# Kernel tuning notes

Measured on AMD Instinct MI355X. Metric: run time of the kernel, lower is better.

Reference implementation:

```python
import jax, jax.numpy as jnp
import numpy as np

BINS = 10  # constructor default


def setup_inputs() -> dict:
    key = jax.random.key(0)
    k1, k2 = jax.random.split(key)
    bs, cla = 262144, 128
    # probabilities strictly inside (0,1) so log terms are finite
    u = jax.random.uniform(k1, (bs, cla), dtype=jnp.float32)
    inputs = 0.01 + 0.98 * u
    # binary 0/1 targets as floats
    targets = jnp.round(jax.random.uniform(k2, (bs, cla), dtype=jnp.float32))
    return {"inputs": inputs, "targets": targets}


def reference(inputs, targets):
    bins = BINS
    tot = jnp.asarray(inputs.size, jnp.float32)  # bs * cla

    # gradient-norm proxy g = |p.detach() - t|, in [0, 1]
    g = jnp.abs(jax.lax.stop_gradient(inputs) - targets)

    # edges are i/bins with the last edge nudged to 1+1e-6, so
    # floor(g*bins) clipped to bins-1 reproduces the per-bin masks exactly
    idx = jnp.clip(jnp.floor(g * bins).astype(jnp.int32), 0, bins - 1)

    # histogram counts per bin (fused scatter-add instead of the Python loop)
    counts = jnp.zeros((bins,), jnp.float32).at[idx.ravel()].add(1.0)

    n = jnp.sum(counts > 0).astype(jnp.float32)  # number of non-empty bins
    w_per_bin = jnp.where(counts > 0, tot / jnp.maximum(counts, 1.0), 0.0)
    weights = w_per_bin[idx] / jnp.maximum(n, 1.0)
    weights = jax.lax.stop_gradient(weights)  # weights built from detached g

    # elementwise binary cross entropy on probabilities
    bce = -(targets * jnp.log(inputs) + (1.0 - targets) * jnp.log1p(-inputs))
    loss = jnp.sum(weights * bce) / tot
    return loss
```

## Files before the change

kernel.cpp:

```cpp
#include <hip/hip_runtime.h>

#define BINS 10

__device__ __forceinline__ void elem(float p, float t,
                                     float* __restrict__ sb,
                                     unsigned int* __restrict__ cw)
{
    float g  = fabsf(p - t);
    float l2 = __log2f(1.0f - g);
    int   bi = (int)(g * 10.0f);
#pragma unroll
    for (int b = 0; b < BINS; ++b) {
        bool hit = (bi == b);
        unsigned long long m = __ballot(hit);
        sb[b] += hit ? l2 : 0.0f;
        cw[b] += (unsigned int)__popcll(m);
    }
}

__device__ __forceinline__ void proc4v(const float4 p, const float4 t,
                                       float* __restrict__ sb,
                                       unsigned int* __restrict__ cw)
{
    elem(p.x, t.x, sb, cw); elem(p.y, t.y, sb, cw);
    elem(p.z, t.z, sb, cw); elem(p.w, t.w, sb, cw);
}

__global__ __launch_bounds__(256, 4) void ghm_partial(
    const float4* __restrict__ p4,
    const float4* __restrict__ t4,
    float* __restrict__ gsum,
    unsigned int* __restrict__ gcnt,
    int n4)
{
    float        sb[BINS];
    unsigned int cw[BINS];
#pragma unroll
    for (int b = 0; b < BINS; ++b) { sb[b] = 0.0f; cw[b] = 0u; }

    const int tid    = threadIdx.x;
    const int start  = blockIdx.x * blockDim.x + tid;
    const int stride = gridDim.x * blockDim.x;
    const int ngrp   = n4 / (4 * stride);

    int i = start;
    for (int grp = 0; grp < ngrp; ++grp, i += 4 * stride) {
        float4 P0 = p4[i];
        float4 T0 = t4[i];
        float4 P1 = p4[i + stride];
        float4 T1 = t4[i + stride];
        float4 P2 = p4[i + 2 * stride];
        float4 T2 = t4[i + 2 * stride];
        float4 P3 = p4[i + 3 * stride];
        float4 T3 = t4[i + 3 * stride];
        __builtin_amdgcn_sched_barrier(0);
        proc4v(P0, T0, sb, cw);
        proc4v(P1, T1, sb, cw);
        proc4v(P2, T2, sb, cw);
        proc4v(P3, T3, sb, cw);
    }
    for (int j = start + ngrp * 4 * stride; j < n4; j += stride) {
        float4 p = p4[j], t = t4[j];
        proc4v(p, t, sb, cw);
    }

    __shared__ float        redS[BINS];
    __shared__ unsigned int redC[BINS];
    if (tid < BINS) { redS[tid] = 0.0f; redC[tid] = 0u; }
    __syncthreads();

    const int lane = tid & 63;
#pragma unroll
    for (int b = 0; b < BINS; ++b) {
        float s = sb[b];
#pragma unroll
        for (int off = 32; off > 0; off >>= 1) s += __shfl_down(s, off);
        if (lane == 0) {
            atomicAdd(&redS[b], s);
            atomicAdd(&redC[b], cw[b]);
        }
    }
    __syncthreads();
    if (tid < BINS) {
        atomicAdd(&gsum[tid], redS[tid]);
        atomicAdd(&gcnt[tid], redC[tid]);
    }
}

__global__ void ghm_finalize(const float* __restrict__ gsum,
                             const unsigned int* __restrict__ gcnt,
                             float* __restrict__ out)
{
    if (threadIdx.x == 0 && blockIdx.x == 0) {
        int n = 0;
#pragma unroll
        for (int b = 0; b < BINS; ++b) n += (gcnt[b] > 0u) ? 1 : 0;
        float nn = (float)(n > 0 ? n : 1);
        float acc = 0.0f;
#pragma unroll
        for (int b = 0; b < BINS; ++b) {
            if (gcnt[b] > 0u)
                acc += gsum[b] / ((float)gcnt[b] * nn);
        }
        out[0] = -0.6931471805599453f * acc;
    }
}

extern "C" void kernel_launch(void* const* d_in, const int* in_sizes, int n_in,
                              void* d_out, int out_size, void* d_ws, size_t ws_size,
                              hipStream_t stream)
{
    const float* p = (const float*)d_in[0];
    const float* t = (const float*)d_in[1];
    const int n  = in_sizes[0];
    const int n4 = n >> 2;

    float*        gsum = (float*)d_ws;
    unsigned int* gcnt = (unsigned int*)((char*)d_ws + BINS * sizeof(float));

    hipMemsetAsync(d_ws, 0, BINS * (sizeof(float) + sizeof(unsigned int)), stream);

    const int threads = 256;
    const int blocks  = 2048;
    ghm_partial<<<blocks, threads, 0, stream>>>(
        (const float4*)p, (const float4*)t, gsum, gcnt, n4);

    ghm_finalize<<<1, 64, 0, stream>>>(gsum, gcnt, (float*)d_out);
}
```

Before: 290.6 us.

## Replace per-bin ballot accumulation with lane-private shared-memory histogram atomics

Each element now does two LDS atomic adds into a histogram indexed by bin and lane, replacing the unrolled loop over all ten bins with a ballot, popcount and conditional add per bin. This removes roughly ten compare/ballot/add steps per element and the register pressure of twenty accumulators. The cost is two shared-memory atomics per element, with the four waves of a block contending on the same lane slots, plus a final shuffle reduction over the lane histograms.

New measurement: 632.6 us. 118% more time.

```diff
diff --git a/kernel.cpp b/kernel.cpp
--- a/kernel.cpp
+++ b/kernel.cpp
@@ -2,28 +2,25 @@
 
 #define BINS 10
 
-__device__ __forceinline__ void elem(float p, float t,
-                                     float* __restrict__ sb,
-                                     unsigned int* __restrict__ cw)
+
+__device__ __forceinline__ void elem(float p, float t, int lane,
+                                     float* __restrict__ hs,
+                                     unsigned int* __restrict__ hc)
 {
     float g  = fabsf(p - t);
     float l2 = __log2f(1.0f - g);
     int   bi = (int)(g * 10.0f);
-#pragma unroll
-    for (int b = 0; b < BINS; ++b) {
-        bool hit = (bi == b);
-        unsigned long long m = __ballot(hit);
-        sb[b] += hit ? l2 : 0.0f;
-        cw[b] += (unsigned int)__popcll(m);
-    }
+    int  idx = (bi << 6) + lane;
+    atomicAdd(hs + idx, l2);
+    atomicAdd(hc + idx, 1u);
 }
 
-__device__ __forceinline__ void proc4v(const float4 p, const float4 t,
-                                       float* __restrict__ sb,
-                                       unsigned int* __restrict__ cw)
+__device__ __forceinline__ void proc4v(const float4 p, const float4 t, int lane,
+                                       float* __restrict__ hs,
+                                       unsigned int* __restrict__ hc)
 {
-    elem(p.x, t.x, sb, cw); elem(p.y, t.y, sb, cw);
-    elem(p.z, t.z, sb, cw); elem(p.w, t.w, sb, cw);
+    elem(p.x, t.x, lane, hs, hc); elem(p.y, t.y, lane, hs, hc);
+    elem(p.z, t.z, lane, hs, hc); elem(p.w, t.w, lane, hs, hc);
 }
 
 __global__ __launch_bounds__(256, 4) void ghm_partial(
@@ -33,12 +30,18 @@
     unsigned int* __restrict__ gcnt,
     int n4)
 {
-    float        sb[BINS];
-    unsigned int cw[BINS];
-#pragma unroll
-    for (int b = 0; b < BINS; ++b) { sb[b] = 0.0f; cw[b] = 0u; }
+    __shared__ float        hsum[BINS * 64];
+    __shared__ unsigned int hcnt[BINS * 64];
 
-    const int tid    = threadIdx.x;
+    const int tid  = threadIdx.x;
+    const int lane = tid & 63;
+
+    for (int k = tid; k < BINS * 64; k += blockDim.x) {
+        hsum[k] = 0.0f;
+        hcnt[k] = 0u;
+    }
+    __syncthreads();
+
     const int start  = blockIdx.x * blockDim.x + tid;
     const int stride = gridDim.x * blockDim.x;
     const int ngrp   = n4 / (4 * stride);
@@ -54,36 +57,33 @@
         float4 P3 = p4[i + 3 * stride];
         float4 T3 = t4[i + 3 * stride];
         __builtin_amdgcn_sched_barrier(0);
-        proc4v(P0, T0, sb, cw);
-        proc4v(P1, T1, sb, cw);
-        proc4v(P2, T2, sb, cw);
-        proc4v(P3, T3, sb, cw);
+        proc4v(P0, T0, lane, hsum, hcnt);
+        proc4v(P1, T1, lane, hsum, hcnt);
+        proc4v(P2, T2, lane, hsum, hcnt);
+        proc4v(P3, T3, lane, hsum, hcnt);
     }
     for (int j = start + ngrp * 4 * stride; j < n4; j += stride) {
         float4 p = p4[j], t = t4[j];
-        proc4v(p, t, sb, cw);
+        proc4v(p, t, lane, hsum, hcnt);
     }
 
-    __shared__ float        redS[BINS];
-    __shared__ unsigned int redC[BINS];
-    if (tid < BINS) { redS[tid] = 0.0f; redC[tid] = 0u; }
     __syncthreads();
 
-    const int lane = tid & 63;
+    if (tid < 64) {
 #pragma unroll
-    for (int b = 0; b < BINS; ++b) {
-        float s = sb[b];
+        for (int b = 0; b < BINS; ++b) {
+            float        s = hsum[(b << 6) + lane];
+            unsigned int c = hcnt[(b << 6) + lane];
 #pragma unroll
-        for (int off = 32; off > 0; off >>= 1) s += __shfl_down(s, off);
-        if (lane == 0) {
-            atomicAdd(&redS[b], s);
-            atomicAdd(&redC[b], cw[b]);
+            for (int off = 32; off > 0; off >>= 1) {
+                s += __shfl_down(s, off);
+                c += __shfl_down(c, off);
+            }
+            if (lane == 0) {
+                atomicAdd(&gsum[b], s);
+                atomicAdd(&gcnt[b], c);
+            }
         }
-    }
-    __syncthreads();
-    if (tid < BINS) {
-        atomicAdd(&gsum[tid], redS[tid]);
-        atomicAdd(&gcnt[tid], redC[tid]);
     }
 }
 
```
